# Performance work log

Hardware: AMD Instinct MI355X
Metric: run time of the kernel (lower is better)

The kernel has to match this reference:

```python
import jax, jax.numpy as jnp
import numpy as np

KS = 3        # opt.kernel_size
B = 8         # batch
T = 512       # total_length (frames)
CQ = 126      # motion channels
CK = 80       # music channels
H = 128       # hid_c
SLOPE = 0.2   # lrelu slope in ConvBlock
INF = jnp.float32(1e30)


def _conv_block(x, w, b):
    # x: [B, Cin, T]; w: [Cout, Cin, KS]; reflect pad, stride 1, lrelu
    xp = jnp.pad(x, ((0, 0), (0, 0), (1, 1)), mode='reflect')
    y = jax.lax.conv_general_dilated(xp, w, (1,), 'VALID',
                                     dimension_numbers=('NCH', 'OIH', 'NCH'))
    return jax.nn.leaky_relu(y + b[None, :, None], SLOPE)


def _encode(x, params):
    for w, b in params:
        x = _conv_block(x, w, b)
    return x  # [B, H, T]


def _dtw_single(d, L):
    # d: [M, N] cost matrix, L: scalar int valid length. Returns 0/1 path matrix.
    M, N = d.shape
    jcol = jnp.arange(N)
    # row 0: cumulative along j, predecessor is 'left' (choice 1)
    row0 = jnp.cumsum(d[0])
    ch0 = jnp.where(jcol == 0, -1, 1).astype(jnp.int32)

    def row_step(prev_row, d_row):
        p_diag = jnp.concatenate([jnp.full((1,), INF), prev_row[:-1]])

        def inner(left, xs):
            pd, pu, dij, j = xs
            m = jnp.minimum(jnp.minimum(pd, left), pu)
            # tie-break order matches numpy code: diag, then left, then up
            choice = jnp.where(pd == m, 0, jnp.where(left == m, 1, 2)).astype(jnp.int32)
            cost = m + dij
            cost = jnp.where(j == 0, pu + dij, cost)      # first column: from up
            choice = jnp.where(j == 0, 2, choice)
            return cost, (cost, choice)

        _, (crow, chrow) = jax.lax.scan(inner, INF, (p_diag, prev_row, d_row, jcol))
        return crow, chrow

    _, chs = jax.lax.scan(row_step, row0, d[1:])
    choices = jnp.concatenate([ch0[None], chs], axis=0)  # [M, N]

    path01 = jnp.zeros((M, N), jnp.float32).at[L - 1, L - 1].set(1.0)

    def bt_step(carry, _):
        ix, iy, p = carry
        active = (ix > 0) | (iy > 0)
        c = choices[ix, iy]
        nix = jnp.where(c == 0, ix - 1, jnp.where(c == 1, ix, ix - 1))
        niy = jnp.where(c == 0, iy - 1, jnp.where(c == 1, iy - 1, iy))
        nix = jnp.where(active, nix, ix)
        niy = jnp.where(active, niy, iy)
        p = p.at[nix, niy].set(jnp.where(active, 1.0, p[nix, niy]))
        return (nix, niy, p), None

    (_, _, path01), _ = jax.lax.scan(bt_step, (L - 1, L - 1, path01), None,
                                     length=2 * M - 2)
    return path01


def setup_inputs() -> dict:
    key = jax.random.key(0)
    ks = jax.random.split(key, 16)

    def w(k, o, i):
        return jax.random.normal(k, (o, i, KS), jnp.float32) * np.float32(np.sqrt(2.0 / (i * KS)))

    inp = {
        'vec': jax.random.normal(ks[0], (B, CQ, T), jnp.float32),
        'music': jax.random.normal(ks[1], (B, CK, T), jnp.float32),
        'real_length': jax.random.randint(ks[2], (B,), T // 2, T + 1, jnp.int32),
        'qw1': w(ks[3], CQ, CQ), 'qb1': jnp.zeros((CQ,), jnp.float32),
        'qw2': w(ks[4], H, CQ),  'qb2': jnp.zeros((H,), jnp.float32),
        'qw3': w(ks[5], H, H),   'qb3': jnp.zeros((H,), jnp.float32),
        'kw1': w(ks[6], CK, CK), 'kb1': jnp.zeros((CK,), jnp.float32),
        'kw2': w(ks[7], H, CK),  'kb2': jnp.zeros((H,), jnp.float32),
        'kw3': w(ks[8], H, H),   'kb3': jnp.zeros((H,), jnp.float32),
    }
    return inp


def reference(vec, music, real_length, qw1, qb1, qw2, qb2, qw3, qb3,
              kw1, kb1, kw2, kb2, kw3, kb3):
    # conv encoders (ConvBlock x3 each)
    q = _encode(vec, [(qw1, qb1), (qw2, qb2), (qw3, qb3)])    # [B, H, T]
    k = _encode(music, [(kw1, kb1), (kw2, kb2), (kw3, kb3)])  # [B, H, T]
    qf = q.transpose(0, 2, 1)  # [B, N, H] motion latent
    kf = k.transpose(0, 2, 1)  # [B, M, H] music latent
    # Euclidean_dist(music_feat=kf, motion_feat=qf): dist[b, m, n] = ||kf[b,m]-qf[b,n]||
    diff = kf[:, :, None, :] - qf[:, None, :, :]              # [B, M, N, H]
    dist = jnp.sqrt(jnp.sum(diff * diff, axis=-1))            # [B, M, N]
    dist = (dist - dist.min()) / (dist.max() - dist.min())    # global min-max norm
    path01 = jax.vmap(_dtw_single)(dist, real_length)         # [B, M, N]
    return (path01, dist)
```

## Files before the change

### kernel.cpp

```cpp
#include <hip/hip_runtime.h>
#include <hip/hip_bf16.h>

#define T_LEN 512
#define BATCH 8
#define HID 128
#define NSTEP 576

__global__ void repack_w_kernel(const float* __restrict__ in,
                                float* __restrict__ out, int n)
{
    int i = blockIdx.x * blockDim.x + threadIdx.x;
    if (i < n) {
        float a = in[i * 3 + 0], b = in[i * 3 + 1], c = in[i * 3 + 2];
        *reinterpret_cast<float4*>(out + i * 4) = make_float4(a, b, c, 0.0f);
    }
}

__global__ __launch_bounds__(512) void conv_block_kernel(
    const float* __restrict__ x, const float* __restrict__ wp,
    const float* __restrict__ bias, float* __restrict__ y,
    int Cin, int Cout)
{
    __shared__ float xs[128 * 66];
    const int b   = blockIdx.z;
    const int t0  = blockIdx.x * 64;
    const int tid = threadIdx.x;
    const int tl  = tid & 63;

    const float* xb = x + (size_t)b * Cin * T_LEN;
    for (int idx = tid; idx < Cin * 66; idx += 512) {
        int ci = idx / 66;
        int tt = idx - ci * 66;
        int g  = t0 + tt - 1;
        g = (g < 0) ? 1 : (g >= T_LEN ? T_LEN - 2 : g);
        xs[idx] = xb[ci * T_LEN + g];
    }
    __syncthreads();

    const int wave = __builtin_amdgcn_readfirstlane(tid >> 6);
    const int co0  = blockIdx.y * 16 + 2 * wave;
    if (co0 < Cout) {
        const float* __restrict__ wq0 = wp + (size_t)co0 * Cin * 4;
        const float* __restrict__ wq1 = wq0 + Cin * 4;
        float acc0 = 0.0f, acc1 = 0.0f;
#pragma unroll 4
        for (int ci = 0; ci < Cin; ++ci) {
            float xm = xs[ci * 66 + tl];
            float x0 = xs[ci * 66 + tl + 1];
            float xp = xs[ci * 66 + tl + 2];
            const float4 w0 = *reinterpret_cast<const float4*>(wq0 + ci * 4);
            const float4 w1 = *reinterpret_cast<const float4*>(wq1 + ci * 4);
            acc0 = fmaf(w0.x, xm, acc0);
            acc0 = fmaf(w0.y, x0, acc0);
            acc0 = fmaf(w0.z, xp, acc0);
            acc1 = fmaf(w1.x, xm, acc1);
            acc1 = fmaf(w1.y, x0, acc1);
            acc1 = fmaf(w1.z, xp, acc1);
        }
        float v0 = acc0 + bias[co0];
        float v1 = acc1 + bias[co0 + 1];
        v0 = (v0 >= 0.0f) ? v0 : 0.2f * v0;
        v1 = (v1 >= 0.0f) ? v1 : 0.2f * v1;
        y[((size_t)b * Cout + co0) * T_LEN + t0 + tl]     = v0;
        y[((size_t)b * Cout + co0 + 1) * T_LEN + t0 + tl] = v1;
    }
}

__global__ __launch_bounds__(256) void dist_kernel(
    const float* __restrict__ q, const float* __restrict__ k,
    float* __restrict__ dist, unsigned* __restrict__ mm)
{
    __shared__ __align__(16) float ks[HID * 32];
    __shared__ __align__(16) float qs[HID * 32];
    __shared__ float red[8];

    const int b  = blockIdx.z;
    const int m0 = blockIdx.y * 32;
    const int n0 = blockIdx.x * 32;
    const int tid = threadIdx.x;

    const float* qb = q + (size_t)b * HID * T_LEN;
    const float* kb = k + (size_t)b * HID * T_LEN;

    for (int idx = tid; idx < HID * 32; idx += 256) {
        int h = idx >> 5, c = idx & 31;
        ks[idx] = kb[h * T_LEN + m0 + c];
        qs[idx] = qb[h * T_LEN + n0 + c];
    }
    __syncthreads();

    const int nn = tid & 31;
    const int mq = (tid >> 5) * 4;

    float a0 = 0.f, a1 = 0.f, a2 = 0.f, a3 = 0.f;
    for (int h = 0; h < HID; ++h) {
        float qv = qs[h * 32 + nn];
        const float4 kv = *reinterpret_cast<const float4*>(&ks[h * 32 + mq]);
        float d0 = kv.x - qv, d1 = kv.y - qv, d2 = kv.z - qv, d3 = kv.w - qv;
        a0 = fmaf(d0, d0, a0);
        a1 = fmaf(d1, d1, a1);
        a2 = fmaf(d2, d2, a2);
        a3 = fmaf(d3, d3, a3);
    }
    float v0 = sqrtf(a0), v1 = sqrtf(a1), v2 = sqrtf(a2), v3 = sqrtf(a3);

    float* drow = dist + ((size_t)b * T_LEN + m0 + mq) * T_LEN + n0 + nn;
    drow[0 * T_LEN] = v0;
    drow[1 * T_LEN] = v1;
    drow[2 * T_LEN] = v2;
    drow[3 * T_LEN] = v3;

    float mnv = fminf(fminf(v0, v1), fminf(v2, v3));
    float mxv = fmaxf(fmaxf(v0, v1), fmaxf(v2, v3));
#pragma unroll
    for (int off = 32; off >= 1; off >>= 1) {
        mnv = fminf(mnv, __shfl_xor(mnv, off, 64));
        mxv = fmaxf(mxv, __shfl_xor(mxv, off, 64));
    }
    int wid = tid >> 6;
    if ((tid & 63) == 0) { red[wid * 2] = mnv; red[wid * 2 + 1] = mxv; }
    __syncthreads();
    if (tid == 0) {
        float mn = fminf(fminf(red[0], red[2]), fminf(red[4], red[6]));
        float mx = fmaxf(fmaxf(red[1], red[3]), fmaxf(red[5], red[7]));
        atomicMin(&mm[0], __float_as_uint(mn));
        atomicMax(&mm[1], __float_as_uint(mx));
    }
}

__global__ __launch_bounds__(512) void norm_shear_kernel(
    float* __restrict__ dist, float* __restrict__ dsk,
    const unsigned* __restrict__ mm)
{
    __shared__ float tile[64][65];
    const float mn  = __uint_as_float(mm[0]);
    const float rng = __uint_as_float(mm[1]) - mn;
    const int b  = blockIdx.z;
    const int m0 = blockIdx.y * 64;
    const int n0 = blockIdx.x * 64;
    const int tid  = threadIdx.x;
    const int lane = tid & 63;
    const int wv   = tid >> 6;

    float* D = dist + (size_t)b * T_LEN * T_LEN;
#pragma unroll
    for (int r = 0; r < 8; ++r) {
        int lm = wv + r * 8;
        float v = (D[(m0 + lm) * T_LEN + n0 + lane] - mn) / rng;
        D[(m0 + lm) * T_LEN + n0 + lane] = v;
        tile[lm][lane] = v;
    }
    __syncthreads();

    float* dskb = dsk + (size_t)b * NSTEP * T_LEN;
    const int tbase = n0 + (m0 >> 3);
#pragma unroll
    for (int it = 0; it < 9; ++it) {
        int t_local = wv + it * 8;
        int ln = t_local - (lane >> 3);
        if (t_local <= 70 && ln >= 0 && ln < 64)
            dskb[(size_t)(tbase + t_local) * T_LEN + m0 + lane] = tile[lane][ln];
    }
}

#define DTW_STEP(T, DA, DB) do {                                              \
    int j = (T) - p;                                                          \
    float u_top = __shfl_up(L[7], 1, 64);                                     \
    float d_top = __shfl_up(prevL7, 1, 64);                                   \
    prevL7 = L[7];                                                            \
    if ((unsigned)j < 512u) {                                                 \
        float dvs[8] = {DA.x, DA.y, DA.z, DA.w, DB.x, DB.y, DB.z, DB.w};      \
        int sh = (j & 15) * 2;                                                \
        float cur, oldL, prevrow;                                             \
        unsigned ch;                                                          \
        if (p == 0) {                                                         \
            cur = (j == 0) ? dvs[0] : (L[0] + dvs[0]); ch = 1u;               \
        } else if (j == 0) {                                                  \
            cur = u_top + dvs[0]; ch = 2u;                                    \
        } else {                                                              \
            float pd = d_top, lf = L[0], pu = u_top;                          \
            float m = fminf(fminf(pd, lf), pu);                               \
            ch = (pd == m) ? 0u : ((lf == m) ? 1u : 2u);                      \
            cur = m + dvs[0];                                                 \
        }                                                                     \
        oldL = L[0]; L[0] = cur; prevrow = cur; pk[0] |= ch << sh;            \
        _Pragma("unroll")                                                     \
        for (int u = 1; u < 8; ++u) {                                         \
            if (j == 0) { cur = prevrow + dvs[u]; ch = 2u; }                  \
            else {                                                            \
                float pd = oldL, lf = L[u], pu = prevrow;                     \
                float m = fminf(fminf(pd, lf), pu);                           \
                ch = (pd == m) ? 0u : ((lf == m) ? 1u : 2u);                  \
                cur = m + dvs[u];                                             \
            }                                                                 \
            oldL = L[u]; L[u] = cur; prevrow = cur; pk[u] |= ch << sh;        \
        }                                                                     \
        if ((j & 15) == 15) {                                                 \
            int w4 = (j >> 4) * 4;                                            \
            *reinterpret_cast<uint4*>(&cho[p * 256 + w4]) =                   \
                make_uint4(pk[0], pk[1], pk[2], pk[3]);                       \
            *reinterpret_cast<uint4*>(&cho[p * 256 + 128 + w4]) =             \
                make_uint4(pk[4], pk[5], pk[6], pk[7]);                       \
            pk[0] = pk[1] = pk[2] = pk[3] = 0u;                               \
            pk[4] = pk[5] = pk[6] = pk[7] = 0u;                               \
        }                                                                     \
    }                                                                         \
} while (0)

__device__ __forceinline__ float4 ld4d(const float* dskb, int t, int off) {
    return *reinterpret_cast<const float4*>(dskb + (size_t)t * T_LEN + off);
}

__global__ __launch_bounds__(64) void dtw_wave_kernel(
    const float* __restrict__ dsk, const int* __restrict__ rlen,
    float* __restrict__ path)
{
    __shared__ unsigned cho[512 * 32];

    const int b  = blockIdx.x;
    const int p  = threadIdx.x;
    const int r0 = p * 8;
    const float* dskb = dsk + (size_t)b * NSTEP * T_LEN;

    float L[8];
    float prevL7 = 1e30f;
#pragma unroll
    for (int u = 0; u < 8; ++u) L[u] = 1e30f;
    unsigned pk[8] = {0u, 0u, 0u, 0u, 0u, 0u, 0u, 0u};

    float4 P0[8], P1[8];
#pragma unroll
    for (int u = 0; u < 8; ++u) {
        P0[u] = ld4d(dskb, u, r0);
        P1[u] = ld4d(dskb, u, r0 + 4);
    }

    for (int t0 = 0; t0 < NSTEP; t0 += 8) {
#pragma unroll
        for (int u = 0; u < 8; ++u) {
            int t  = t0 + u;
            int tn = t + 8; tn = (tn < NSTEP) ? tn : (NSTEP - 1);
            float4 Na = ld4d(dskb, tn, r0);
            float4 Nb = ld4d(dskb, tn, r0 + 4);
            DTW_STEP(t, P0[u], P1[u]);
            P0[u] = Na; P1[u] = Nb;
        }
    }

    __syncthreads();

    if (p == 0) {
        int Lr = rlen[b];
        int ix = Lr - 1, iy = Lr - 1;
        float* po = path + (size_t)b * T_LEN * T_LEN;
        po[ix * T_LEN + iy] = 1.0f;
        while (ix > 0 || iy > 0) {
            uint4 tw = *reinterpret_cast<const uint4*>(
                &cho[((ix >> 2) * 32 + (iy >> 4)) * 4]);
            int tr = ix >> 2, tc = iy >> 4;
            while (true) {
                int sel = ix & 3;
                unsigned wvv = (sel & 2) ? ((sel & 1) ? tw.w : tw.z)
                                         : ((sel & 1) ? tw.y : tw.x);
                int c = (wvv >> ((iy & 15) * 2)) & 3;
                ix -= (c != 1);
                iy -= (c != 2);
                po[ix * T_LEN + iy] = 1.0f;
                if (!(ix > 0 || iy > 0)) break;
                if ((ix >> 2) != tr || (iy >> 4) != tc) break;
            }
        }
    }
}

extern "C" void kernel_launch(void* const* d_in, const int* in_sizes, int n_in,
                              void* d_out, int out_size, void* d_ws, size_t ws_size,
                              hipStream_t stream)
{
    (void)in_sizes; (void)n_in; (void)out_size; (void)ws_size;

    const float* vec   = (const float*)d_in[0];
    const float* music = (const float*)d_in[1];
    const int*   rlen  = (const int*)  d_in[2];
    const float* qw1 = (const float*)d_in[3];  const float* qb1 = (const float*)d_in[4];
    const float* qw2 = (const float*)d_in[5];  const float* qb2 = (const float*)d_in[6];
    const float* qw3 = (const float*)d_in[7];  const float* qb3 = (const float*)d_in[8];
    const float* kw1 = (const float*)d_in[9];  const float* kb1 = (const float*)d_in[10];
    const float* kw2 = (const float*)d_in[11]; const float* kb2 = (const float*)d_in[12];
    const float* kw3 = (const float*)d_in[13]; const float* kb3 = (const float*)d_in[14];

    float* out = (float*)d_out;
    const size_t mat_elems = (size_t)BATCH * T_LEN * T_LEN;
    float* path_out = out;
    float* dist_out = out + mat_elems;

    char* ws = (char*)d_ws;
    const size_t bufB = (size_t)BATCH * HID * T_LEN * sizeof(float);
    float* dsk = (float*)ws;
    float* qA = (float*)(ws + 0 * bufB);
    float* qB = (float*)(ws + 1 * bufB);
    float* kA = (float*)(ws + 2 * bufB);
    float* kB = (float*)(ws + 3 * bufB);
    char* wr = ws + 4 * bufB;
    float* qw1p = (float*)(wr);
    float* qw2p = (float*)(wr + 254016);
    float* qw3p = (float*)(wr + 512064);
    float* kw1p = (float*)(wr + 774208);
    float* kw2p = (float*)(wr + 876608);
    float* kw3p = (float*)(wr + 1040448);
    unsigned* mm = (unsigned*)(ws + 9691200);

    hipMemsetAsync(path_out, 0, mat_elems * sizeof(float), stream);
    hipMemsetAsync(mm, 0xFF, 4, stream);
    hipMemsetAsync(mm + 1, 0x00, 4, stream);

    repack_w_kernel<<<(126 * 126 + 255) / 256, 256, 0, stream>>>(qw1, qw1p, 126 * 126);
    repack_w_kernel<<<(128 * 126 + 255) / 256, 256, 0, stream>>>(qw2, qw2p, 128 * 126);
    repack_w_kernel<<<(128 * 128 + 255) / 256, 256, 0, stream>>>(qw3, qw3p, 128 * 128);
    repack_w_kernel<<<(80 * 80 + 255) / 256, 256, 0, stream>>>(kw1, kw1p, 80 * 80);
    repack_w_kernel<<<(128 * 80 + 255) / 256, 256, 0, stream>>>(kw2, kw2p, 128 * 80);
    repack_w_kernel<<<(128 * 128 + 255) / 256, 256, 0, stream>>>(kw3, kw3p, 128 * 128);

    dim3 cb(512);
    conv_block_kernel<<<dim3(8, 8, 8), cb, 0, stream>>>(vec, qw1p, qb1, qA, 126, 126);
    conv_block_kernel<<<dim3(8, 8, 8), cb, 0, stream>>>(qA,  qw2p, qb2, qB, 126, 128);
    conv_block_kernel<<<dim3(8, 8, 8), cb, 0, stream>>>(qB,  qw3p, qb3, qA, 128, 128);
    conv_block_kernel<<<dim3(8, 5, 8), cb, 0, stream>>>(music, kw1p, kb1, kA, 80, 80);
    conv_block_kernel<<<dim3(8, 8, 8), cb, 0, stream>>>(kA,   kw2p, kb2, kB, 80, 128);
    conv_block_kernel<<<dim3(8, 8, 8), cb, 0, stream>>>(kB,   kw3p, kb3, kA, 128, 128);

    dist_kernel<<<dim3(16, 16, 8), dim3(256), 0, stream>>>(qA, kA, dist_out, mm);

    norm_shear_kernel<<<dim3(8, 8, 8), dim3(512), 0, stream>>>(dist_out, dsk, mm);

    dtw_wave_kernel<<<dim3(BATCH), dim3(64), 0, stream>>>(dsk, rlen, path_out);
}
```

Before: 624.3 us.

## Stage DTW cost diagonals through LDS with async global-to-LDS loads

The DTW wavefront kernel now double-buffers groups of 8 sheared diagonals in shared memory using global_load_lds, and each step reads its values from LDS one diagonal ahead. To make those LDS reads conflict-free, the shear kernel writes a permuted column layout. Previously each thread kept 16 float4 register prefetches from global memory. Separately, the six weight-repack kernels are merged into one launch with a compact output layout. The intent is to take global load latency and register pressure off the serial single-wave DTW critical path. The cost is extra LDS use and hand-written vmcnt waits, which are fragile.

```diff
diff --git a/kernel.cpp b/kernel.cpp
--- a/kernel.cpp
+++ b/kernel.cpp
@@ -6,14 +6,23 @@
 #define HID 128
 #define NSTEP 576
 
-__global__ void repack_w_kernel(const float* __restrict__ in,
-                                float* __restrict__ out, int n)
-{
-    int i = blockIdx.x * blockDim.x + threadIdx.x;
-    if (i < n) {
-        float a = in[i * 3 + 0], b = in[i * 3 + 1], c = in[i * 3 + 2];
-        *reinterpret_cast<float4*>(out + i * 4) = make_float4(a, b, c, 0.0f);
-    }
+__global__ __launch_bounds__(256) void repack_all_kernel(
+    const float* __restrict__ s0, const float* __restrict__ s1,
+    const float* __restrict__ s2, const float* __restrict__ s3,
+    const float* __restrict__ s4, const float* __restrict__ s5,
+    float* __restrict__ out)
+{
+    int i = blockIdx.x * 256 + threadIdx.x;
+    const float* src; int li; float* dst;
+    if      (i < 15876) { src = s0; li = i;         dst = out;          }
+    else if (i < 32004) { src = s1; li = i - 15876; dst = out + 63504;  }
+    else if (i < 48388) { src = s2; li = i - 32004; dst = out + 128016; }
+    else if (i < 54788) { src = s3; li = i - 48388; dst = out + 193552; }
+    else if (i < 65028) { src = s4; li = i - 54788; dst = out + 219152; }
+    else if (i < 81412) { src = s5; li = i - 65028; dst = out + 260112; }
+    else return;
+    float a = src[li * 3], b = src[li * 3 + 1], c = src[li * 3 + 2];
+    *reinterpret_cast<float4*>(dst + li * 4) = make_float4(a, b, c, 0.0f);
 }
 
 __global__ __launch_bounds__(512) void conv_block_kernel(
@@ -154,44 +163,64 @@
 
     float* dskb = dsk + (size_t)b * NSTEP * T_LEN;
     const int tbase = n0 + (m0 >> 3);
+    const int pidx  = (lane & 7) * 64 + (m0 >> 3) + (lane >> 3);
 #pragma unroll
     for (int it = 0; it < 9; ++it) {
         int t_local = wv + it * 8;
         int ln = t_local - (lane >> 3);
         if (t_local <= 70 && ln >= 0 && ln < 64)
-            dskb[(size_t)(tbase + t_local) * T_LEN + m0 + lane] = tile[lane][ln];
-    }
-}
-
-#define DTW_STEP(T, DA, DB) do {                                              \
+            dskb[(size_t)(tbase + t_local) * T_LEN + pidx] = tile[lane][ln];
+    }
+}
+
+__device__ __forceinline__ void gload_lds16(const float* g, float* l) {
+    __builtin_amdgcn_global_load_lds(
+        (const __attribute__((address_space(1))) unsigned*)g,
+        (__attribute__((address_space(3))) unsigned*)l, 16, 0, 0);
+}
+
+#define STAGE(GG, BUFI) do {                                                  \
+    const float* gsrc = dskb + (size_t)(GG) * 8 * T_LEN;                      \
+    _Pragma("unroll")                                                         \
+    for (int rr = 0; rr < 8; ++rr) {                                          \
+        gload_lds16(gsrc + rr * T_LEN +   0 + p * 4, &dstage[BUFI][rr][0]);   \
+        gload_lds16(gsrc + rr * T_LEN + 256 + p * 4, &dstage[BUFI][rr][256]); \
+    }                                                                         \
+} while (0)
+
+#define PREF(ARR, BUFI, ROWN) do {                                            \
+    _Pragma("unroll")                                                         \
+    for (int u = 0; u < 8; ++u) ARR[u] = dstage[BUFI][ROWN][u * 64 + p];      \
+} while (0)
+
+#define DTW_STEP_A(T, ARR) do {                                               \
     int j = (T) - p;                                                          \
     float u_top = __shfl_up(L[7], 1, 64);                                     \
     float d_top = __shfl_up(prevL7, 1, 64);                                   \
     prevL7 = L[7];                                                            \
     if ((unsigned)j < 512u) {                                                 \
-        float dvs[8] = {DA.x, DA.y, DA.z, DA.w, DB.x, DB.y, DB.z, DB.w};      \
         int sh = (j & 15) * 2;                                                \
         float cur, oldL, prevrow;                                             \
         unsigned ch;                                                          \
         if (p == 0) {                                                         \
-            cur = (j == 0) ? dvs[0] : (L[0] + dvs[0]); ch = 1u;               \
+            cur = (j == 0) ? ARR[0] : (L[0] + ARR[0]); ch = 1u;               \
         } else if (j == 0) {                                                  \
-            cur = u_top + dvs[0]; ch = 2u;                                    \
+            cur = u_top + ARR[0]; ch = 2u;                                    \
         } else {                                                              \
             float pd = d_top, lf = L[0], pu = u_top;                          \
             float m = fminf(fminf(pd, lf), pu);                               \
             ch = (pd == m) ? 0u : ((lf == m) ? 1u : 2u);                      \
-            cur = m + dvs[0];                                                 \
+            cur = m + ARR[0];                                                 \
         }                                                                     \
         oldL = L[0]; L[0] = cur; prevrow = cur; pk[0] |= ch << sh;            \
         _Pragma("unroll")                                                     \
         for (int u = 1; u < 8; ++u) {                                         \
-            if (j == 0) { cur = prevrow + dvs[u]; ch = 2u; }                  \
+            if (j == 0) { cur = prevrow + ARR[u]; ch = 2u; }                  \
             else {                                                            \
                 float pd = oldL, lf = L[u], pu = prevrow;                     \
                 float m = fminf(fminf(pd, lf), pu);                           \
                 ch = (pd == m) ? 0u : ((lf == m) ? 1u : 2u);                  \
-                cur = m + dvs[u];                                             \
+                cur = m + ARR[u];                                             \
             }                                                                 \
             oldL = L[u]; L[u] = cur; prevrow = cur; pk[u] |= ch << sh;        \
         }                                                                     \
@@ -207,19 +236,15 @@
     }                                                                         \
 } while (0)
 
-__device__ __forceinline__ float4 ld4d(const float* dskb, int t, int off) {
-    return *reinterpret_cast<const float4*>(dskb + (size_t)t * T_LEN + off);
-}
-
 __global__ __launch_bounds__(64) void dtw_wave_kernel(
     const float* __restrict__ dsk, const int* __restrict__ rlen,
     float* __restrict__ path)
 {
+    __shared__ float dstage[2][8][512];
     __shared__ unsigned cho[512 * 32];
 
-    const int b  = blockIdx.x;
-    const int p  = threadIdx.x;
-    const int r0 = p * 8;
+    const int b = blockIdx.x;
+    const int p = threadIdx.x;
     const float* dskb = dsk + (size_t)b * NSTEP * T_LEN;
 
     float L[8];
@@ -228,23 +253,31 @@
     for (int u = 0; u < 8; ++u) L[u] = 1e30f;
     unsigned pk[8] = {0u, 0u, 0u, 0u, 0u, 0u, 0u, 0u};
 
-    float4 P0[8], P1[8];
-#pragma unroll
-    for (int u = 0; u < 8; ++u) {
-        P0[u] = ld4d(dskb, u, r0);
-        P1[u] = ld4d(dskb, u, r0 + 4);
-    }
-
-    for (int t0 = 0; t0 < NSTEP; t0 += 8) {
-#pragma unroll
-        for (int u = 0; u < 8; ++u) {
-            int t  = t0 + u;
-            int tn = t + 8; tn = (tn < NSTEP) ? tn : (NSTEP - 1);
-            float4 Na = ld4d(dskb, tn, r0);
-            float4 Nb = ld4d(dskb, tn, r0 + 4);
-            DTW_STEP(t, P0[u], P1[u]);
-            P0[u] = Na; P1[u] = Nb;
+    STAGE(0, 0);
+    STAGE(1, 1);
+    asm volatile("s_waitcnt vmcnt(16)" ::: "memory");
+
+    float da[8], db[8];
+    PREF(da, 0, 0);
+
+    for (int g = 0; g < 72; ++g) {
+        const int cbuf = g & 1, nbuf = cbuf ^ 1;
+        const int t0 = g * 8;
+        PREF(db, cbuf, 1); DTW_STEP_A(t0 + 0, da);
+        PREF(da, cbuf, 2); DTW_STEP_A(t0 + 1, db);
+        PREF(db, cbuf, 3); DTW_STEP_A(t0 + 2, da);
+        PREF(da, cbuf, 4); DTW_STEP_A(t0 + 3, db);
+        PREF(db, cbuf, 5); DTW_STEP_A(t0 + 4, da);
+        PREF(da, cbuf, 6); DTW_STEP_A(t0 + 5, db);
+        PREF(db, cbuf, 7); DTW_STEP_A(t0 + 6, da);
+        DTW_STEP_A(t0 + 7, db);
+        if (g + 2 < 72) {
+            STAGE(g + 2, cbuf);
+            asm volatile("s_waitcnt vmcnt(16)" ::: "memory");
+        } else {
+            asm volatile("s_waitcnt vmcnt(0)" ::: "memory");
         }
+        if (g + 1 < 72) PREF(da, nbuf, 0);
     }
 
     __syncthreads();
@@ -301,25 +334,21 @@
     float* qB = (float*)(ws + 1 * bufB);
     float* kA = (float*)(ws + 2 * bufB);
     float* kB = (float*)(ws + 3 * bufB);
-    char* wr = ws + 4 * bufB;
-    float* qw1p = (float*)(wr);
-    float* qw2p = (float*)(wr + 254016);
-    float* qw3p = (float*)(wr + 512064);
-    float* kw1p = (float*)(wr + 774208);
-    float* kw2p = (float*)(wr + 876608);
-    float* kw3p = (float*)(wr + 1040448);
+    float* wrep = (float*)(ws + 4 * bufB);
+    float* qw1p = wrep;
+    float* qw2p = wrep + 63504;
+    float* qw3p = wrep + 128016;
+    float* kw1p = wrep + 193552;
+    float* kw2p = wrep + 219152;
+    float* kw3p = wrep + 260112;
     unsigned* mm = (unsigned*)(ws + 9691200);
 
     hipMemsetAsync(path_out, 0, mat_elems * sizeof(float), stream);
     hipMemsetAsync(mm, 0xFF, 4, stream);
     hipMemsetAsync(mm + 1, 0x00, 4, stream);
 
-    repack_w_kernel<<<(126 * 126 + 255) / 256, 256, 0, stream>>>(qw1, qw1p, 126 * 126);
-    repack_w_kernel<<<(128 * 126 + 255) / 256, 256, 0, stream>>>(qw2, qw2p, 128 * 126);
-    repack_w_kernel<<<(128 * 128 + 255) / 256, 256, 0, stream>>>(qw3, qw3p, 128 * 128);
-    repack_w_kernel<<<(80 * 80 + 255) / 256, 256, 0, stream>>>(kw1, kw1p, 80 * 80);
-    repack_w_kernel<<<(128 * 80 + 255) / 256, 256, 0, stream>>>(kw2, kw2p, 128 * 80);
-    repack_w_kernel<<<(128 * 128 + 255) / 256, 256, 0, stream>>>(kw3, kw3p, 128 * 128);
+    repack_all_kernel<<<dim3((81412 + 255) / 256), dim3(256), 0, stream>>>(
+        qw1, qw2, qw3, kw1, kw2, kw3, wrep);
 
     dim3 cb(512);
     conv_block_kernel<<<dim3(8, 8, 8), cb, 0, stream>>>(vec, qw1p, qb1, qA, 126, 126);
```

Result: no change. 636.0 us (+1.9%).
